# Optimization experiments

Measured on AMD Instinct MI355X. Metric: run time of the kernel, lower is better.

The kernel has to match this reference:

```python
import jax, jax.numpy as jnp
import numpy as np

THRESHOLD = 0.5
NEG_POS_RATIO = 3
CONF_WEIGHT = 1.0
VAR = (0.1, 0.1, 0.2, 0.2)
EPS_LOG = 1e-5


def _center_to_corner(p):
    cx, cy, w, h = p[:, 0], p[:, 1], p[:, 2], p[:, 3]
    return jnp.stack([cx - w / 2, cy - h / 2, cx + w / 2, cy + h / 2], axis=1)


def _iou(gt, pr):  # gt [M,4] corners, pr [P,4] corners -> [M,P]
    lt = jnp.maximum(gt[:, None, :2], pr[None, :, :2])
    rb = jnp.minimum(gt[:, None, 2:], pr[None, :, 2:])
    wh = jnp.clip(rb - lt, 0.0)
    inter = wh[..., 0] * wh[..., 1]
    area_g = (gt[:, 2] - gt[:, 0]) * (gt[:, 3] - gt[:, 1])
    area_p = (pr[:, 2] - pr[:, 0]) * (pr[:, 3] - pr[:, 1])
    return inter / (area_g[:, None] + area_p[None, :] - inter + 1e-10)


def _match_one(gt_boxes, priors_corner):
    # standard SSD matching: per-prior best GT if IoU >= threshold, else -1;
    # each GT additionally claims its best prior.
    iou = _iou(gt_boxes, priors_corner)            # [M,P]
    best_gt = jnp.argmax(iou, axis=0)              # [P]
    best_iou = jnp.max(iou, axis=0)                # [P]
    truth = jnp.where(best_iou >= THRESHOLD, best_gt, -1)
    best_prior = jnp.argmax(iou, axis=1)           # [M]
    truth = truth.at[best_prior].set(jnp.arange(gt_boxes.shape[0]))
    return truth


def _encode(matched_gt, priors):
    # matched_gt [B,P,4] corners, priors [P,4] center form -> [B,P,4]
    g_cx = (matched_gt[..., 0] + matched_gt[..., 2]) / 2
    g_cy = (matched_gt[..., 1] + matched_gt[..., 3]) / 2
    g_w = matched_gt[..., 2] - matched_gt[..., 0]
    g_h = matched_gt[..., 3] - matched_gt[..., 1]
    p_cx, p_cy, p_w, p_h = priors[:, 0], priors[:, 1], priors[:, 2], priors[:, 3]
    enc_cx = (g_cx - p_cx) / (p_w * VAR[0])
    enc_cy = (g_cy - p_cy) / (p_h * VAR[1])
    enc_w = jnp.log(g_w / p_w + EPS_LOG) / VAR[2]
    enc_h = jnp.log(g_h / p_h + EPS_LOG) / VAR[3]
    return jnp.stack([enc_cx, enc_cy, enc_w, enc_h], axis=-1)


def setup_inputs() -> dict:
    key = jax.random.key(0)
    ks = jax.random.split(key, 7)
    B, P, C, M = 64, 8732, 81, 20
    pred_loc = jax.random.normal(ks[0], (B, P, 4), jnp.float32)
    pred_conf = jax.random.normal(ks[1], (B, P, C), jnp.float32)
    # priors in center form (cx, cy, w, h)
    p_c = jax.random.uniform(ks[2], (P, 2), jnp.float32)
    p_wh = jax.random.uniform(ks[3], (P, 2), jnp.float32, minval=0.05, maxval=0.5)
    priors = jnp.concatenate([p_c, p_wh], axis=1)
    # GT boxes in corner form, guaranteed valid (x2>x1, y2>y1)
    g_c = jax.random.uniform(ks[4], (B, M, 2), jnp.float32, minval=0.2, maxval=0.8)
    g_wh = jax.random.uniform(ks[5], (B, M, 2), jnp.float32, minval=0.05, maxval=0.3)
    targets_boxes = jnp.concatenate([g_c - g_wh / 2, g_c + g_wh / 2], axis=-1)
    targets_labels = jax.random.randint(ks[6], (B, M), 1, C, jnp.int32)
    return {"pred_loc": pred_loc, "pred_conf": pred_conf, "priors": priors,
            "targets_boxes": targets_boxes, "targets_labels": targets_labels}


def reference(pred_loc, pred_conf, priors, targets_boxes, targets_labels):
    B, P, C = pred_conf.shape
    priors_corner = _center_to_corner(priors)
    truth = jax.vmap(lambda g: _match_one(g, priors_corner))(targets_boxes)  # [B,P]
    pos_mask = truth != -1
    safe = jnp.maximum(truth, 0)
    matched_gt = jax.vmap(lambda t, s: t[s])(targets_boxes, safe)            # [B,P,4]
    target_conf = jnp.where(pos_mask,
                            jax.vmap(lambda l, s: l[s])(targets_labels, safe), 0)

    # localization loss: smooth-L1 (beta=1), sum over matched priors, / batch
    enc = _encode(matched_gt, priors)
    d = pred_loc - enc
    ad = jnp.abs(d)
    sl1 = jnp.where(ad < 1.0, 0.5 * d * d, ad - 0.5)
    loc_loss = jnp.sum(sl1 * pos_mask[..., None]) / B

    # confidence loss with hard negative mining (3:1, double-argsort rank trick)
    logp = jax.nn.log_softmax(pred_conf, axis=-1)                            # [B,P,C]
    ce = -jnp.take_along_axis(logp, target_conf[..., None], axis=-1)[..., 0]  # [B,P]
    ce_neg = jnp.where(pos_mask, 0.0, ce)
    order = jnp.argsort(-ce_neg, axis=1)
    rank = jnp.argsort(order, axis=1)
    pos_num = jnp.sum(pos_mask, axis=1, keepdims=True)
    neg_num = jnp.minimum(NEG_POS_RATIO * pos_num, P - 1)
    neg_mask = rank < neg_num
    prior_mask = pos_mask | neg_mask
    conf_loss = jnp.sum(ce * prior_mask) / jnp.sum(prior_mask) / B * CONF_WEIGHT
    return (loc_loss, conf_loss)
```

## Files before the change

### kernel.cpp

```cpp
#include <hip/hip_runtime.h>
#include <hip/hip_bf16.h>

#define B_   64
#define P_   8732
#define C_   81
#define M_   20
#define BP_  (B_*P_)
#define CEB  128
#define CETH 512
#define NV   (CEB*C_/4)
#define NCH  9
#define SBLK 1024

__global__ __launch_bounds__(256) void iou_kernel(
    const float* __restrict__ priors, const float* __restrict__ tboxes,
    int* __restrict__ truth, unsigned long long* __restrict__ bestc,
    int* __restrict__ pos_cnt, float* __restrict__ pos_sum,
    float* __restrict__ accums, int* __restrict__ done)
{
    const int b = blockIdx.y;
    const int tid = threadIdx.x;

    if (blockIdx.x == 0 && b == 0) {
        if (tid < B_) { pos_cnt[tid] = 0; pos_sum[tid] = 0.f; }
        if (tid >= B_ && tid < B_ + 3) accums[tid - B_] = 0.f;
        if (tid == B_ + 3) *done = 0;
    }

    __shared__ float s_gt[M_][4];
    __shared__ float s_ga[M_];
    __shared__ float s_red[M_][4];
    __shared__ int   s_redp[M_][4];

    if (tid < M_*4) ((float*)s_gt)[tid] = tboxes[b*M_*4 + tid];
    __syncthreads();
    if (tid < M_) s_ga[tid] = (s_gt[tid][2]-s_gt[tid][0]) * (s_gt[tid][3]-s_gt[tid][1]);
    __syncthreads();

    float lb[M_]; int lp[M_];
    #pragma unroll
    for (int m=0;m<M_;++m){ lb[m] = -1.0f; lp[m] = 0x7FFFFFFF; }

    const float4* pr4 = (const float4*)priors;
    const int p0 = blockIdx.x * 1024;
    const int pend = min(p0 + 1024, P_);
    for (int p = p0 + tid; p < pend; p += 256) {
        float4 pc = pr4[p];
        float px0 = pc.x - pc.z*0.5f, py0 = pc.y - pc.w*0.5f;
        float px1 = pc.x + pc.z*0.5f, py1 = pc.y + pc.w*0.5f;
        float pa = pc.z * pc.w;
        float best = -1.0f; int bg = 0;
        #pragma unroll
        for (int m=0;m<M_;++m){
            float ix0 = fmaxf(s_gt[m][0], px0);
            float iy0 = fmaxf(s_gt[m][1], py0);
            float ix1 = fminf(s_gt[m][2], px1);
            float iy1 = fminf(s_gt[m][3], py1);
            float iw = fmaxf(ix1-ix0, 0.f), ih = fmaxf(iy1-iy0, 0.f);
            float inter = iw*ih;
            float iou = inter / (s_ga[m] + pa - inter + 1e-10f);
            if (iou > best) { best = iou; bg = m; }
            if (iou > lb[m]) { lb[m] = iou; lp[m] = p; }
        }
        truth[(size_t)b*P_ + p] = (best >= 0.5f) ? bg : -1;
    }

    const int lane = tid & 63, wid = tid >> 6;
    #pragma unroll
    for (int m=0;m<M_;++m){
        float v = lb[m]; int ip = lp[m];
        for (int off=32; off; off>>=1){
            float ov = __shfl_down(v, off); int op = __shfl_down(ip, off);
            if (ov > v || (ov == v && op < ip)) { v = ov; ip = op; }
        }
        if (lane == 0) { s_red[m][wid] = v; s_redp[m][wid] = ip; }
    }
    __syncthreads();
    if (tid < M_) {
        const int m = tid;
        float v = s_red[m][0]; int ip = s_redp[m][0];
        for (int w=1; w<4; ++w){
            float ov = s_red[m][w]; int op = s_redp[m][w];
            if (ov > v || (ov == v && op < ip)) { v = ov; ip = op; }
        }
        bestc[(b*M_ + m)*NCH + blockIdx.x] =
            ((unsigned long long)__float_as_uint(v) << 32) | (unsigned)(P_ - 1 - ip);
    }
}

__global__ __launch_bounds__(CETH) void ce_loc_kernel(
    const float* __restrict__ pred_conf, const float* __restrict__ pred_loc,
    const float* __restrict__ priors, const float* __restrict__ tboxes,
    const int* __restrict__ tlabels, const int* __restrict__ truth,
    const unsigned long long* __restrict__ bestc,
    float* __restrict__ ce_neg, int* __restrict__ pos_cnt,
    float* __restrict__ pos_sum, float* __restrict__ accums)
{
    __shared__ float sc[CEB * C_];
    __shared__ int   s_fp[2][M_];
    __shared__ int   s_pos[2];
    __shared__ float s_psum[2];
    __shared__ float s_loc[CETH/64];
    const int tid = threadIdx.x;
    const int base = blockIdx.x * CEB;
    const int b0 = base / P_;

    const float4* src4 = (const float4*)(pred_conf + (size_t)base * C_);
    float4* dst4 = (float4*)sc;
#if __has_builtin(__builtin_amdgcn_global_load_lds)
    #pragma unroll
    for (int k = 0; k < NV / CETH; ++k) {
        const int i = tid + k * CETH;
        __builtin_amdgcn_global_load_lds(
            (const __attribute__((address_space(1))) void*)(src4 + i),
            (__attribute__((address_space(3))) void*)(dst4 + i), 16, 0, 0);
    }
    if (tid < NV - (NV / CETH) * CETH) {
        const int i = (NV / CETH) * CETH + tid;
        __builtin_amdgcn_global_load_lds(
            (const __attribute__((address_space(1))) void*)(src4 + i),
            (__attribute__((address_space(3))) void*)(dst4 + i), 16, 0, 0);
    }
#else
    for (int i = tid; i < NV; i += CETH) dst4[i] = src4[i];
#endif

    if (tid < 2*M_) {
        const int j = tid / M_, m = tid - j*M_;
        const int bb = b0 + j;
        int p = -1;
        if (bb < B_) {
            const unsigned long long* src = &bestc[(bb*M_ + m)*NCH];
            unsigned long long best = src[0];
            #pragma unroll
            for (int c = 1; c < NCH; ++c) { unsigned long long kk = src[c]; if (kk > best) best = kk; }
            p = P_ - 1 - (int)(unsigned)(best & 0xFFFFFFFFu);
        }
        s_fp[j][m] = p;
    }
    if (tid < 2) { s_pos[tid] = 0; s_psum[tid] = 0.f; }
    __syncthreads();

    const int r = tid >> 2;
    const int q = tid & 3;
    const float* row = &sc[r * C_];
    const int c0 = q * 20 + (q > 0 ? 1 : 0);
    const int cn = (q == 0) ? 21 : 20;
    float mx = -1e30f;
    for (int c = 0; c < cn; ++c) mx = fmaxf(mx, row[c0 + c]);
    mx = fmaxf(mx, __shfl_xor(mx, 1));
    mx = fmaxf(mx, __shfl_xor(mx, 2));
    float s = 0.f;
    for (int c = 0; c < cn; ++c) s += __expf(row[c0 + c] - mx);
    s += __shfl_xor(s, 1);
    s += __shfl_xor(s, 2);

    float locacc = 0.f;
    if (q == 0) {
        const int bp = base + r;
        const int b = bp / P_;
        const int p = bp - b * P_;
        const int jb = b - b0;
        int t = truth[bp];
        #pragma unroll
        for (int m = 0; m < M_; ++m)
            if (s_fp[jb][m] == p) t = m;
        const int cls = (t >= 0) ? tlabels[b*M_ + t] : 0;
        const float ce = mx + __logf(s) - row[cls];
        if (t >= 0) {
            atomicAdd(&s_pos[jb], 1);
            atomicAdd(&s_psum[jb], ce);
            ce_neg[bp] = 0.f;
            float4 pc = ((const float4*)priors)[p];
            float4 g  = ((const float4*)tboxes)[b*M_ + t];
            float gcx = (g.x+g.z)*0.5f, gcy = (g.y+g.w)*0.5f;
            float gw = g.z - g.x, gh = g.w - g.y;
            float e0 = (gcx - pc.x) / (pc.z * 0.1f);
            float e1 = (gcy - pc.y) / (pc.w * 0.1f);
            float e2 = __logf(gw / pc.z + 1e-5f) * 5.0f;
            float e3 = __logf(gh / pc.w + 1e-5f) * 5.0f;
            float4 pl = ((const float4*)pred_loc)[bp];
            float d0 = pl.x-e0, d1 = pl.y-e1, d2 = pl.z-e2, d3 = pl.w-e3;
            float a0 = fabsf(d0), a1 = fabsf(d1), a2 = fabsf(d2), a3 = fabsf(d3);
            locacc = (a0<1.f ? 0.5f*d0*d0 : a0-0.5f)
                   + (a1<1.f ? 0.5f*d1*d1 : a1-0.5f)
                   + (a2<1.f ? 0.5f*d2*d2 : a2-0.5f)
                   + (a3<1.f ? 0.5f*d3*d3 : a3-0.5f);
        } else {
            ce_neg[bp] = ce;
        }
    }
    for (int off=32; off; off>>=1) locacc += __shfl_down(locacc, off);
    if ((tid & 63) == 0) s_loc[tid>>6] = locacc;
    __syncthreads();
    if (tid == 0) {
        float a = 0.f;
        #pragma unroll
        for (int w = 0; w < CETH/64; ++w) a += s_loc[w];
        if (a != 0.f) atomicAdd(&accums[0], a);
    }
    if (tid < 2) {
        const int br = b0 + tid;
        if (br < B_ && s_pos[tid] > 0) {
            atomicAdd(&pos_cnt[br], s_pos[tid]);
            atomicAdd(&pos_sum[br], s_psum[tid]);
        }
    }
}

__global__ __launch_bounds__(SBLK) void select_kernel(
    const float* __restrict__ ce_neg, const int* __restrict__ pos_cnt,
    const float* __restrict__ pos_sum, float* __restrict__ accums,
    int* __restrict__ done, float* __restrict__ out)
{
    const int b = blockIdx.x; const int tid = threadIdx.x;
    const int lane = tid & 63;
    __shared__ float cl[P_];
    __shared__ unsigned hist[256];
    __shared__ unsigned s_sel, s_prefix, s_remk, s_cntgt;
    __shared__ float s_r1[SBLK/64];
    __shared__ int s_last;

    const float* cerow = ce_neg + (size_t)b * P_;
    if (tid < 256) hist[tid] = 0u;
    if (tid == 0) s_sel = 0u;
    __syncthreads();

    for (int i = tid; i < P_; i += SBLK) {
        const unsigned bin = __float_as_uint(cerow[i]) >> 24;
        unsigned long long todo = __ballot(1);
        while (todo) {
            const int src = (int)__ffsll(todo) - 1;
            const unsigned lead = __shfl(bin, src);
            const unsigned long long mset = __ballot(bin == lead);
            if (lane == src) atomicAdd(&hist[lead], (unsigned)__popcll(mset));
            todo &= ~mset;
        }
    }
    __syncthreads();
    const int pos = pos_cnt[b];
    const unsigned k = (unsigned)min(3 * pos, P_ - 1);
    if (tid == 0) {
        unsigned acc = 0, chosen = 0;
        for (int bin = 255; bin >= 0; --bin) {
            const unsigned c = hist[bin];
            if (acc + c >= k) { chosen = (unsigned)bin; break; }
            acc += c;
        }
        s_prefix = chosen << 24; s_remk = k - acc; s_cntgt = acc;
    }
    __syncthreads();
    const unsigned c3 = s_prefix >> 24;

    float gsum = 0.f;
    for (int i = tid; i < P_; i += SBLK) {
        const float v = cerow[i];
        const unsigned byt = __float_as_uint(v) >> 24;
        if (byt > c3) gsum += v;
        const bool pred = (byt == c3);
        const unsigned long long mset = __ballot(pred);
        if (pred) {
            const int leader = (int)__ffsll(mset) - 1;
            unsigned bse;
            if (lane == leader) bse = atomicAdd(&s_sel, (unsigned)__popcll(mset));
            bse = __shfl(bse, leader);
            cl[bse + __popcll(mset & ((1ull << lane) - 1ull))] = v;
        }
    }
    __syncthreads();
    const int L = (int)s_sel;

    for (int pass = 2; pass >= 0; --pass) {
        if (tid < 256) hist[tid] = 0u;
        __syncthreads();
        const unsigned prefix = s_prefix;
        const int shift = pass * 8;
        const unsigned pmask = 0xFFFFFFFFu << (shift + 8);
        for (int i = tid; i < L; i += SBLK) {
            const unsigned u = __float_as_uint(cl[i]);
            if ((u & pmask) == prefix) atomicAdd(&hist[(u >> shift) & 0xFFu], 1u);
        }
        __syncthreads();
        if (tid == 0) {
            unsigned remk = s_remk, acc = 0, chosen = 0;
            for (int bin = 255; bin >= 0; --bin) {
                const unsigned c = hist[bin];
                if (acc + c >= remk) { chosen = (unsigned)bin; break; }
                acc += c;
            }
            s_cntgt += acc; s_remk = remk - acc; s_prefix = prefix | (chosen << shift);
        }
        __syncthreads();
    }

    const unsigned Tbits = s_prefix;
    const float T = __uint_as_float(Tbits);
    float sgt = gsum;
    for (int i = tid; i < L; i += SBLK) {
        const float v = cl[i];
        if (__float_as_uint(v) > Tbits) sgt += v;
    }
    for (int off=32; off; off>>=1) sgt += __shfl_down(sgt, off);
    if (lane == 0) s_r1[tid>>6] = sgt;
    __syncthreads();
    if (tid == 0) {
        float a = 0.f;
        #pragma unroll
        for (int w = 0; w < SBLK/64; ++w) a += s_r1[w];
        const unsigned sel_eq = s_remk;
        float neg_sum, mc;
        if (Tbits != 0u) { neg_sum = a + (float)sel_eq * T; mc = (float)(pos + (int)k); }
        else             { neg_sum = a;                     mc = (float)(pos + (int)s_cntgt); }
        atomicAdd(&accums[1], pos_sum[b] + neg_sum);
        atomicAdd(&accums[2], mc);
        __threadfence();
        const int old = atomicAdd(done, 1);
        s_last = (old == B_ - 1);
    }
    __syncthreads();
    if (tid == 0 && s_last) {
        const float l  = atomicAdd(&accums[0], 0.f);
        const float cs = atomicAdd(&accums[1], 0.f);
        const float mn = atomicAdd(&accums[2], 0.f);
        out[0] = l / (float)B_;
        out[1] = cs / mn / (float)B_;
    }
}

extern "C" void kernel_launch(void* const* d_in, const int* in_sizes, int n_in,
                              void* d_out, int out_size, void* d_ws, size_t ws_size,
                              hipStream_t stream) {
    (void)in_sizes; (void)n_in; (void)out_size; (void)ws_size;
    const float* pred_loc  = (const float*)d_in[0];
    const float* pred_conf = (const float*)d_in[1];
    const float* priors    = (const float*)d_in[2];
    const float* tboxes    = (const float*)d_in[3];
    const int*   tlabels   = (const int*)d_in[4];
    float* out = (float*)d_out;

    char* ws = (char*)d_ws;
    int*   truth  = (int*)ws;
    float* ce_neg = (float*)(ws + (size_t)BP_ * 4);
    unsigned long long* bestc = (unsigned long long*)(ws + (size_t)BP_ * 8);
    char* tail = ws + (size_t)BP_ * 8 + (size_t)B_*M_*NCH*8;
    int*   pos_cnt = (int*)tail;
    float* pos_sum = (float*)(tail + B_*4);
    float* accums  = (float*)(tail + B_*8);
    int*   done    = (int*)(tail + B_*8 + 12);

    iou_kernel<<<dim3(NCH, B_), 256, 0, stream>>>(priors, tboxes, truth, bestc,
                                                  pos_cnt, pos_sum, accums, done);
    ce_loc_kernel<<<BP_ / CEB, CETH, 0, stream>>>(pred_conf, pred_loc, priors, tboxes,
                                                  tlabels, truth, bestc,
                                                  ce_neg, pos_cnt, pos_sum, accums);
    select_kernel<<<B_, SBLK, 0, stream>>>(ce_neg, pos_cnt, pos_sum, accums, done, out);
}
```

Before: 154.9 us.

## Fuse hard-negative selection into CE kernel via per-row completion counters

```diff
diff --git a/kernel.cpp b/kernel.cpp
--- a/kernel.cpp
+++ b/kernel.cpp
@@ -10,21 +10,19 @@
 #define CETH 512
 #define NV   (CEB*C_/4)
 #define NCH  9
-#define SBLK 1024
 
 __global__ __launch_bounds__(256) void iou_kernel(
     const float* __restrict__ priors, const float* __restrict__ tboxes,
     int* __restrict__ truth, unsigned long long* __restrict__ bestc,
     int* __restrict__ pos_cnt, float* __restrict__ pos_sum,
-    float* __restrict__ accums, int* __restrict__ done)
+    float* __restrict__ accums, int* __restrict__ done, int* __restrict__ row_done)
 {
     const int b = blockIdx.y;
     const int tid = threadIdx.x;
 
     if (blockIdx.x == 0 && b == 0) {
-        if (tid < B_) { pos_cnt[tid] = 0; pos_sum[tid] = 0.f; }
-        if (tid >= B_ && tid < B_ + 3) accums[tid - B_] = 0.f;
-        if (tid == B_ + 3) *done = 0;
+        if (tid < B_) { pos_cnt[tid] = 0; pos_sum[tid] = 0.f; row_done[tid] = 0; }
+        if (tid == B_) { accums[0] = 0.f; accums[1] = 0.f; accums[2] = 0.f; *done = 0; }
     }
 
     __shared__ float s_gt[M_][4];
@@ -88,22 +86,30 @@
     }
 }
 
-__global__ __launch_bounds__(CETH) void ce_loc_kernel(
+__global__ __launch_bounds__(CETH) void ce_sel_kernel(
     const float* __restrict__ pred_conf, const float* __restrict__ pred_loc,
     const float* __restrict__ priors, const float* __restrict__ tboxes,
     const int* __restrict__ tlabels, const int* __restrict__ truth,
     const unsigned long long* __restrict__ bestc,
     float* __restrict__ ce_neg, int* __restrict__ pos_cnt,
-    float* __restrict__ pos_sum, float* __restrict__ accums)
+    float* __restrict__ pos_sum, float* __restrict__ accums,
+    int* __restrict__ done, int* __restrict__ row_done, float* __restrict__ out)
 {
-    __shared__ float sc[CEB * C_];
-    __shared__ int   s_fp[2][M_];
-    __shared__ int   s_pos[2];
-    __shared__ float s_psum[2];
-    __shared__ float s_loc[CETH/64];
+    __shared__ __align__(16) float sc[CEB * C_];
+    __shared__ int      s_fp[2][M_];
+    __shared__ int      s_pos[2];
+    __shared__ float    s_psum[2];
+    __shared__ float    s_loc[CETH/64];
+    __shared__ int      s_run[2];
+    __shared__ unsigned hist[256];
+    __shared__ unsigned s_sel, s_prefix, s_remk, s_cntgt;
+    __shared__ float    s_r1[CETH/64];
+    __shared__ int      s_last;
+
     const int tid = threadIdx.x;
     const int base = blockIdx.x * CEB;
     const int b0 = base / P_;
+    const int b1 = (base + CEB - 1) / P_;
 
     const float4* src4 = (const float4*)(pred_conf + (size_t)base * C_);
     float4* dst4 = (float4*)sc;
@@ -167,10 +173,11 @@
             if (s_fp[jb][m] == p) t = m;
         const int cls = (t >= 0) ? tlabels[b*M_ + t] : 0;
         const float ce = mx + __logf(s) - row[cls];
+        float cev = ce;
         if (t >= 0) {
             atomicAdd(&s_pos[jb], 1);
             atomicAdd(&s_psum[jb], ce);
-            ce_neg[bp] = 0.f;
+            cev = 0.f;
             float4 pc = ((const float4*)priors)[p];
             float4 g  = ((const float4*)tboxes)[b*M_ + t];
             float gcx = (g.x+g.z)*0.5f, gcy = (g.y+g.w)*0.5f;
@@ -186,9 +193,8 @@
                    + (a1<1.f ? 0.5f*d1*d1 : a1-0.5f)
                    + (a2<1.f ? 0.5f*d2*d2 : a2-0.5f)
                    + (a3<1.f ? 0.5f*d3*d3 : a3-0.5f);
-        } else {
-            ce_neg[bp] = ce;
-        }
+        }
+        __hip_atomic_store(&ce_neg[bp], cev, __ATOMIC_RELAXED, __HIP_MEMORY_SCOPE_AGENT);
     }
     for (int off=32; off; off>>=1) locacc += __shfl_down(locacc, off);
     if ((tid & 63) == 0) s_loc[tid>>6] = locacc;
@@ -206,124 +212,132 @@
             atomicAdd(&pos_sum[br], s_psum[tid]);
         }
     }
-}
-
-__global__ __launch_bounds__(SBLK) void select_kernel(
-    const float* __restrict__ ce_neg, const int* __restrict__ pos_cnt,
-    const float* __restrict__ pos_sum, float* __restrict__ accums,
-    int* __restrict__ done, float* __restrict__ out)
-{
-    const int b = blockIdx.x; const int tid = threadIdx.x;
-    const int lane = tid & 63;
-    __shared__ float cl[P_];
-    __shared__ unsigned hist[256];
-    __shared__ unsigned s_sel, s_prefix, s_remk, s_cntgt;
-    __shared__ float s_r1[SBLK/64];
-    __shared__ int s_last;
-
-    const float* cerow = ce_neg + (size_t)b * P_;
-    if (tid < 256) hist[tid] = 0u;
-    if (tid == 0) s_sel = 0u;
-    __syncthreads();
-
-    for (int i = tid; i < P_; i += SBLK) {
-        const unsigned bin = __float_as_uint(cerow[i]) >> 24;
-        unsigned long long todo = __ballot(1);
-        while (todo) {
-            const int src = (int)__ffsll(todo) - 1;
-            const unsigned lead = __shfl(bin, src);
-            const unsigned long long mset = __ballot(bin == lead);
-            if (lane == src) atomicAdd(&hist[lead], (unsigned)__popcll(mset));
-            todo &= ~mset;
-        }
-    }
-    __syncthreads();
-    const int pos = pos_cnt[b];
-    const unsigned k = (unsigned)min(3 * pos, P_ - 1);
-    if (tid == 0) {
-        unsigned acc = 0, chosen = 0;
-        for (int bin = 255; bin >= 0; --bin) {
-            const unsigned c = hist[bin];
-            if (acc + c >= k) { chosen = (unsigned)bin; break; }
-            acc += c;
-        }
-        s_prefix = chosen << 24; s_remk = k - acc; s_cntgt = acc;
-    }
-    __syncthreads();
-    const unsigned c3 = s_prefix >> 24;
-
-    float gsum = 0.f;
-    for (int i = tid; i < P_; i += SBLK) {
-        const float v = cerow[i];
-        const unsigned byt = __float_as_uint(v) >> 24;
-        if (byt > c3) gsum += v;
-        const bool pred = (byt == c3);
-        const unsigned long long mset = __ballot(pred);
-        if (pred) {
-            const int leader = (int)__ffsll(mset) - 1;
-            unsigned bse;
-            if (lane == leader) bse = atomicAdd(&s_sel, (unsigned)__popcll(mset));
-            bse = __shfl(bse, leader);
-            cl[bse + __popcll(mset & ((1ull << lane) - 1ull))] = v;
-        }
-    }
-    __syncthreads();
-    const int L = (int)s_sel;
-
-    for (int pass = 2; pass >= 0; --pass) {
+
+    asm volatile("s_waitcnt vmcnt(0)" ::: "memory");
+    __syncthreads();
+    if (tid < 2) {
+        s_run[tid] = -1;
+        const int br = b0 + tid;
+        const bool spans = (tid == 0) || (b1 != b0);
+        if (spans && br < B_) {
+            const int first = (br * P_) / CEB;
+            const int last  = ((br + 1) * P_ - 1) / CEB;
+            const int old = atomicAdd(&row_done[br], 1);
+            if (old == last - first) s_run[tid] = br;
+        }
+    }
+    __syncthreads();
+
+    #pragma unroll
+    for (int j = 0; j < 2; ++j) {
+        const int b = s_run[j];
+        if (b < 0) continue;
+
+        const float* cerow = ce_neg + (size_t)b * P_;
+        const int lane = tid & 63;
         if (tid < 256) hist[tid] = 0u;
-        __syncthreads();
-        const unsigned prefix = s_prefix;
-        const int shift = pass * 8;
-        const unsigned pmask = 0xFFFFFFFFu << (shift + 8);
-        for (int i = tid; i < L; i += SBLK) {
-            const unsigned u = __float_as_uint(cl[i]);
-            if ((u & pmask) == prefix) atomicAdd(&hist[(u >> shift) & 0xFFu], 1u);
-        }
-        __syncthreads();
+        if (tid == 0) s_sel = 0u;
+        __syncthreads();
+
+        for (int i = tid; i < P_; i += CETH) {
+            const unsigned bin = __float_as_uint(cerow[i]) >> 24;
+            unsigned long long todo = __ballot(1);
+            while (todo) {
+                const int src = (int)__ffsll(todo) - 1;
+                const unsigned lead = __shfl(bin, src);
+                const unsigned long long mset = __ballot(bin == lead);
+                if (lane == src) atomicAdd(&hist[lead], (unsigned)__popcll(mset));
+                todo &= ~mset;
+            }
+        }
+        __syncthreads();
+        const int pos = atomicAdd(&pos_cnt[b], 0);
+        const unsigned k = (unsigned)min(3 * pos, P_ - 1);
         if (tid == 0) {
-            unsigned remk = s_remk, acc = 0, chosen = 0;
+            unsigned acc = 0, chosen = 0;
             for (int bin = 255; bin >= 0; --bin) {
                 const unsigned c = hist[bin];
-                if (acc + c >= remk) { chosen = (unsigned)bin; break; }
+                if (acc + c >= k) { chosen = (unsigned)bin; break; }
                 acc += c;
             }
-            s_cntgt += acc; s_remk = remk - acc; s_prefix = prefix | (chosen << shift);
-        }
-        __syncthreads();
-    }
-
-    const unsigned Tbits = s_prefix;
-    const float T = __uint_as_float(Tbits);
-    float sgt = gsum;
-    for (int i = tid; i < L; i += SBLK) {
-        const float v = cl[i];
-        if (__float_as_uint(v) > Tbits) sgt += v;
-    }
-    for (int off=32; off; off>>=1) sgt += __shfl_down(sgt, off);
-    if (lane == 0) s_r1[tid>>6] = sgt;
-    __syncthreads();
-    if (tid == 0) {
-        float a = 0.f;
-        #pragma unroll
-        for (int w = 0; w < SBLK/64; ++w) a += s_r1[w];
-        const unsigned sel_eq = s_remk;
-        float neg_sum, mc;
-        if (Tbits != 0u) { neg_sum = a + (float)sel_eq * T; mc = (float)(pos + (int)k); }
-        else             { neg_sum = a;                     mc = (float)(pos + (int)s_cntgt); }
-        atomicAdd(&accums[1], pos_sum[b] + neg_sum);
-        atomicAdd(&accums[2], mc);
-        __threadfence();
-        const int old = atomicAdd(done, 1);
-        s_last = (old == B_ - 1);
-    }
-    __syncthreads();
-    if (tid == 0 && s_last) {
-        const float l  = atomicAdd(&accums[0], 0.f);
-        const float cs = atomicAdd(&accums[1], 0.f);
-        const float mn = atomicAdd(&accums[2], 0.f);
-        out[0] = l / (float)B_;
-        out[1] = cs / mn / (float)B_;
+            s_prefix = chosen << 24; s_remk = k - acc; s_cntgt = acc;
+        }
+        __syncthreads();
+        const unsigned c3 = s_prefix >> 24;
+
+        float gsum = 0.f;
+        for (int i = tid; i < P_; i += CETH) {
+            const float v = cerow[i];
+            const unsigned byt = __float_as_uint(v) >> 24;
+            if (byt > c3) gsum += v;
+            const bool pred = (byt == c3);
+            const unsigned long long mset = __ballot(pred);
+            if (pred) {
+                const int leader = (int)__ffsll(mset) - 1;
+                unsigned bse;
+                if (lane == leader) bse = atomicAdd(&s_sel, (unsigned)__popcll(mset));
+                bse = __shfl(bse, leader);
+                sc[bse + __popcll(mset & ((1ull << lane) - 1ull))] = v;
+            }
+        }
+        __syncthreads();
+        const int L = (int)s_sel;
+
+        for (int pass = 2; pass >= 0; --pass) {
+            if (tid < 256) hist[tid] = 0u;
+            __syncthreads();
+            const unsigned prefix = s_prefix;
+            const int shift = pass * 8;
+            const unsigned pmask = 0xFFFFFFFFu << (shift + 8);
+            for (int i = tid; i < L; i += CETH) {
+                const unsigned u = __float_as_uint(sc[i]);
+                if ((u & pmask) == prefix) atomicAdd(&hist[(u >> shift) & 0xFFu], 1u);
+            }
+            __syncthreads();
+            if (tid == 0) {
+                unsigned remk = s_remk, acc = 0, chosen = 0;
+                for (int bin = 255; bin >= 0; --bin) {
+                    const unsigned c = hist[bin];
+                    if (acc + c >= remk) { chosen = (unsigned)bin; break; }
+                    acc += c;
+                }
+                s_cntgt += acc; s_remk = remk - acc; s_prefix = prefix | (chosen << shift);
+            }
+            __syncthreads();
+        }
+
+        const unsigned Tbits = s_prefix;
+        const float T = __uint_as_float(Tbits);
+        float sgt = gsum;
+        for (int i = tid; i < L; i += CETH) {
+            const float v = sc[i];
+            if (__float_as_uint(v) > Tbits) sgt += v;
+        }
+        for (int off=32; off; off>>=1) sgt += __shfl_down(sgt, off);
+        if (lane == 0) s_r1[tid>>6] = sgt;
+        __syncthreads();
+        if (tid == 0) {
+            float a = 0.f;
+            #pragma unroll
+            for (int w = 0; w < CETH/64; ++w) a += s_r1[w];
+            const unsigned sel_eq = s_remk;
+            float neg_sum, mc;
+            if (Tbits != 0u) { neg_sum = a + (float)sel_eq * T; mc = (float)(pos + (int)k); }
+            else             { neg_sum = a;                     mc = (float)(pos + (int)s_cntgt); }
+            atomicAdd(&accums[1], atomicAdd(&pos_sum[b], 0.f) + neg_sum);
+            atomicAdd(&accums[2], mc);
+            const int old = atomicAdd(done, 1);
+            s_last = (old == B_ - 1);
+        }
+        __syncthreads();
+        if (tid == 0 && s_last) {
+            const float l  = atomicAdd(&accums[0], 0.f);
+            const float cs = atomicAdd(&accums[1], 0.f);
+            const float mn = atomicAdd(&accums[2], 0.f);
+            out[0] = l / (float)B_;
+            out[1] = cs / mn / (float)B_;
+        }
+        __syncthreads();
     }
 }
 
@@ -343,15 +357,16 @@
     float* ce_neg = (float*)(ws + (size_t)BP_ * 4);
     unsigned long long* bestc = (unsigned long long*)(ws + (size_t)BP_ * 8);
     char* tail = ws + (size_t)BP_ * 8 + (size_t)B_*M_*NCH*8;
-    int*   pos_cnt = (int*)tail;
-    float* pos_sum = (float*)(tail + B_*4);
-    float* accums  = (float*)(tail + B_*8);
-    int*   done    = (int*)(tail + B_*8 + 12);
+    int*   pos_cnt  = (int*)tail;
+    float* pos_sum  = (float*)(tail + B_*4);
+    float* accums   = (float*)(tail + B_*8);
+    int*   done     = (int*)(tail + B_*8 + 12);
+    int*   row_done = (int*)(tail + B_*8 + 16);
 
     iou_kernel<<<dim3(NCH, B_), 256, 0, stream>>>(priors, tboxes, truth, bestc,
-                                                  pos_cnt, pos_sum, accums, done);
-    ce_loc_kernel<<<BP_ / CEB, CETH, 0, stream>>>(pred_conf, pred_loc, priors, tboxes,
+                                                  pos_cnt, pos_sum, accums, done, row_done);
+    ce_sel_kernel<<<BP_ / CEB, CETH, 0, stream>>>(pred_conf, pred_loc, priors, tboxes,
                                                   tlabels, truth, bestc,
-                                                  ce_neg, pos_cnt, pos_sum, accums);
-    select_kernel<<<B_, SBLK, 0, stream>>>(ce_neg, pos_cnt, pos_sum, accums, done, out);
+                                                  ce_neg, pos_cnt, pos_sum, accums,
+                                                  done, row_done, out);
 }
```

Result: slower. 189.4 us (+22.3%).
